# Kernel optimization log

Measured on AMD Instinct MI355X. Metric: run time of the kernel, lower is better.

## Reference

```python
import jax, jax.numpy as jnp
import numpy as np

K = 8   # kernelsize
S = 4   # kernelstride
P = 0   # kernelpadding


def setup_inputs() -> dict:
    key = jax.random.key(0)
    x = jax.random.normal(key, (16, 3, 512, 512), dtype=jnp.float32)
    return {"x": x}


def reference(x):
    # Original module runs conv2d with an identity (eye) kernel on each
    # (batch, channel) plane separately: that is exactly patch extraction
    # (im2col). conv_general_dilated_patches with 1 input channel produces
    # output channels ordered row-major over the k x k window, identical to
    # the eye-kernel conv's output-channel ordering. Bias is zeros (no-op).
    B, C, H, W = x.shape
    xr = x.reshape(B * C, 1, H, W)
    patches = jax.lax.conv_general_dilated_patches(
        xr, filter_shape=(K, K), window_strides=(S, S),
        padding=[(P, P), (P, P)])  # [B*C, K*K, Ho, Wo]
    Ho, Wo = patches.shape[-2], patches.shape[-1]
    # permute(0,2,3,1) -> reshape(B, C, Ho*Wo, K*K) -> permute(0,2,1,3)
    out = patches.transpose(0, 2, 3, 1)              # [B*C, Ho, Wo, K*K]
    out = out.reshape(B, C, Ho * Wo, K * K)          # [B, C, Ho*Wo, K*K]
    out = out.transpose(0, 2, 1, 3)                  # [B, Ho*Wo, C, K*K]
    return out
```

## Files before the change

### kernel.cpp

```cpp
#include <hip/hip_runtime.h>


namespace {
typedef float f32x4 __attribute__((ext_vector_type(4)));

constexpr int B  = 16;
constexpr int C  = 3;
constexpr int H  = 512;
constexpr int W  = 512;
constexpr int S  = 4;
constexpr int Ho = 127;
constexpr int Wo = 127;
constexpr int P  = Ho * Wo;
constexpr int ROW_PAD = W + 4;
constexpr int LDS_FLOATS = C * 8 * ROW_PAD;
constexpr int IN_F4_PER_C = 8 * W / 4;
constexpr int IN_F4 = C * IN_F4_PER_C;
constexpr int OUT_F4_PER_GROUP = Wo * C * 16;
constexpr int NWG = B * Ho;
constexpr int TPB = 512;
}

__global__ __launch_bounds__(TPB) void
PatchesKernel3D_34892314313629_kernel(const float* __restrict__ x,
                                      float* __restrict__ out) {
    __shared__ float lds[LDS_FLOATS];

    const int bid = (int)blockIdx.x;
    const int logical = (bid & 7) * (NWG / 8) + (bid >> 3);
    const int b  = logical / Ho;
    const int ho = logical - b * Ho;

    const int tid = (int)threadIdx.x;

    const f32x4* __restrict__ x4 = reinterpret_cast<const f32x4*>(x);
    #pragma unroll
    for (int l = tid; l < IN_F4; l += TPB) {
        const int c = l >> 10;
        const int r = l & 1023;
        const size_t src4 =
            ((size_t)((b * C + c) * H + ho * S) * W) / 4 + r;
        const f32x4 v = x4[src4];
        const int row  = r >> 7;
        const int col4 = r & 127;
        *reinterpret_cast<f32x4*>(
            &lds[c * 8 * ROW_PAD + row * ROW_PAD + col4 * 4]) = v;
    }

    __syncthreads();

    f32x4* __restrict__ out4 = reinterpret_cast<f32x4*>(out);
    const size_t out_base4 = ((size_t)(b * P + ho * Wo) * C) * 16;

    for (int o = tid; o < OUT_F4_PER_GROUP; o += TPB) {
        const int j  = o & 15;
        const int q  = o >> 4;
        const int c  = q % 3;
        const int wo = q / 3;
        const int kh  = j >> 1;
        const int kw0 = (j & 1) << 2;
        const f32x4 v = *reinterpret_cast<const f32x4*>(
            &lds[c * 8 * ROW_PAD + kh * ROW_PAD + wo * S + kw0]);
        __builtin_nontemporal_store(v, &out4[out_base4 + o]);
    }
}

extern "C" void kernel_launch(void* const* d_in, const int* in_sizes, int n_in,
                              void* d_out, int out_size, void* d_ws, size_t ws_size,
                              hipStream_t stream) {
    const float* x = (const float*)d_in[0];
    float* out = (float*)d_out;
    PatchesKernel3D_34892314313629_kernel<<<NWG, TPB, 0, stream>>>(x, out);
}
```

Measured before the change: 42.79 us.

## Split patch workgroups per channel and use regular stores

Each workgroup now handles a single (batch, output-row, channel) slab instead of all three channels, so there are three times as many workgroups, each with 256 threads and a third of the LDS. The aim is better occupancy and finer load balancing. The trade-off is that each workgroup's output writes become strided 256-byte chunks (64 floats per patch, with the other channels interleaved) instead of one contiguous run. Nontemporal stores are also replaced with ordinary stores, which changes how the cache handles the large output stream.

```diff
diff --git a/kernel.cpp b/kernel.cpp
--- a/kernel.cpp
+++ b/kernel.cpp
@@ -13,12 +13,11 @@
 constexpr int Wo = 127;
 constexpr int P  = Ho * Wo;
 constexpr int ROW_PAD = W + 4;
-constexpr int LDS_FLOATS = C * 8 * ROW_PAD;
-constexpr int IN_F4_PER_C = 8 * W / 4;
-constexpr int IN_F4 = C * IN_F4_PER_C;
-constexpr int OUT_F4_PER_GROUP = Wo * C * 16;
-constexpr int NWG = B * Ho;
-constexpr int TPB = 512;
+constexpr int LDS_FLOATS = 8 * ROW_PAD;
+constexpr int IN_F4  = 8 * W / 4;
+constexpr int OUT_F4 = Wo * 16;
+constexpr int NWG = B * Ho * C;
+constexpr int TPB = 256;
 }
 
 __global__ __launch_bounds__(TPB) void
@@ -28,40 +27,36 @@
 
     const int bid = (int)blockIdx.x;
     const int logical = (bid & 7) * (NWG / 8) + (bid >> 3);
-    const int b  = logical / Ho;
-    const int ho = logical - b * Ho;
+    const int c  = logical % C;
+    const int t  = logical / C;
+    const int ho = t % Ho;
+    const int b  = t / Ho;
 
     const int tid = (int)threadIdx.x;
 
     const f32x4* __restrict__ x4 = reinterpret_cast<const f32x4*>(x);
+    const size_t src_base4 = ((size_t)((b * C + c) * H + ho * S) * W) / 4;
     #pragma unroll
     for (int l = tid; l < IN_F4; l += TPB) {
-        const int c = l >> 10;
-        const int r = l & 1023;
-        const size_t src4 =
-            ((size_t)((b * C + c) * H + ho * S) * W) / 4 + r;
-        const f32x4 v = x4[src4];
-        const int row  = r >> 7;
-        const int col4 = r & 127;
-        *reinterpret_cast<f32x4*>(
-            &lds[c * 8 * ROW_PAD + row * ROW_PAD + col4 * 4]) = v;
+        const f32x4 v = x4[src_base4 + l];
+        const int row  = l >> 7;
+        const int col4 = l & 127;
+        *reinterpret_cast<f32x4*>(&lds[row * ROW_PAD + col4 * 4]) = v;
     }
 
     __syncthreads();
 
     f32x4* __restrict__ out4 = reinterpret_cast<f32x4*>(out);
-    const size_t out_base4 = ((size_t)(b * P + ho * Wo) * C) * 16;
+    const size_t out_base4 = ((size_t)(b * P + ho * Wo) * C + c) * 16;
 
-    for (int o = tid; o < OUT_F4_PER_GROUP; o += TPB) {
+    for (int o = tid; o < OUT_F4; o += TPB) {
         const int j  = o & 15;
-        const int q  = o >> 4;
-        const int c  = q % 3;
-        const int wo = q / 3;
+        const int wo = o >> 4;
         const int kh  = j >> 1;
         const int kw0 = (j & 1) << 2;
         const f32x4 v = *reinterpret_cast<const f32x4*>(
-            &lds[c * 8 * ROW_PAD + kh * ROW_PAD + wo * S + kw0]);
-        __builtin_nontemporal_store(v, &out4[out_base4 + o]);
+            &lds[kh * ROW_PAD + wo * S + kw0]);
+        out4[out_base4 + wo * 48 + j] = v;
     }
 }
 
```

Result: no change. 42.32 us (-1.1%).
